# Kernel optimization log

Hardware: AMD Instinct MI355X
Metric: run time of the kernel (lower is better)

Reference implementation:

```python
import jax, jax.numpy as jnp
import numpy as np

EPS = 1e-8  # matches F.cosine_similarity eps


def setup_inputs() -> dict:
    key = jax.random.key(0)
    k1, k2 = jax.random.split(key)
    N, D = 4096, 256
    z1 = jax.random.normal(k1, (N, D), dtype=jnp.float32)
    z2 = jax.random.normal(k2, (N, D), dtype=jnp.float32)
    log_temperature = jnp.asarray(np.log(0.07), dtype=jnp.float32)
    return {"z1": z1, "z2": z2, "log_temperature": log_temperature}


def reference(z1, z2, log_temperature):
    N = z1.shape[0]
    z = jnp.concatenate([z1, z2], axis=0)                      # (2N, D)
    # cosine similarity: normalize once, then a single GEMM
    norm = jnp.maximum(jnp.linalg.norm(z, axis=-1, keepdims=True), EPS)
    zn = z / norm
    sim = zn @ zn.T                                            # (2N, 2N)
    diag = jnp.eye(2 * N, dtype=bool)
    sim = jnp.where(diag, -jnp.inf, sim)
    targets = jnp.concatenate([jnp.arange(N, 2 * N), jnp.arange(0, N)])
    logits = sim / jnp.exp(log_temperature)
    logp = jax.nn.log_softmax(logits, axis=-1)                 # (2N, 2N)
    loss = -jnp.mean(jnp.take_along_axis(logp, targets[:, None], axis=1))
    correct = jnp.sum(jnp.argmax(sim, axis=1) == targets).astype(jnp.float32) / 2.0
    return (loss, correct)
```

## Files before the change

kernel.cpp:

```cpp
#include <hip/hip_runtime.h>
#include <hip/hip_fp16.h>

#define NTOT 8192
#define NHALF 4096
#define DIM 256
#define LOG2E 1.4426950408889634f
#define NEG_BIG -1e30f
#define COLSPLIT 8
#define BM 128
#define BN 64
#define CPB (NTOT / COLSPLIT)

typedef _Float16 half8 __attribute__((ext_vector_type(8)));
typedef float floatx4 __attribute__((ext_vector_type(4)));

__global__ __launch_bounds__(256) void k_normalize(const float* __restrict__ z1,
                                                   const float* __restrict__ z2,
                                                   __half* __restrict__ zn) {
  int row = blockIdx.x * 4 + (threadIdx.x >> 6);
  int lane = threadIdx.x & 63;
  const float* src = (row < NHALF) ? (z1 + (size_t)row * DIM)
                                   : (z2 + (size_t)(row - NHALF) * DIM);
  float4 v = ((const float4*)src)[lane];
  float ss = v.x * v.x + v.y * v.y + v.z * v.z + v.w * v.w;
#pragma unroll
  for (int m = 1; m < 64; m <<= 1) ss += __shfl_xor(ss, m);
  float inv = 1.0f / fmaxf(sqrtf(ss), 1e-8f);
  __half2 h0, h1;
  h0.x = __float2half_rn(v.x * inv);
  h0.y = __float2half_rn(v.y * inv);
  h1.x = __float2half_rn(v.z * inv);
  h1.y = __float2half_rn(v.w * inv);
  __half2* dst = (__half2*)(zn + (size_t)row * DIM + lane * 4);
  dst[0] = h0;
  dst[1] = h1;
}

__global__ __launch_bounds__(256) void k_tsim(const __half* __restrict__ zn,
                                              float* __restrict__ tsim) {
  int row = blockIdx.x * 4 + (threadIdx.x >> 6);
  int lane = threadIdx.x & 63;
  int tgt = (row < NHALF) ? row + NHALF : row - NHALF;
  const __half2* a = (const __half2*)(zn + (size_t)row * DIM);
  const __half2* b = (const __half2*)(zn + (size_t)tgt * DIM);
  float s = 0.f;
#pragma unroll
  for (int j = 0; j < 2; j++) {
    float2 xf = __half22float2(a[lane * 2 + j]);
    float2 yf = __half22float2(b[lane * 2 + j]);
    s += xf.x * yf.x + xf.y * yf.y;
  }
#pragma unroll
  for (int m = 1; m < 64; m <<= 1) s += __shfl_xor(s, m);
  if (lane == 0) tsim[row] = s;
}

__global__ __launch_bounds__(256, 2) void k_main(const __half* __restrict__ zn,
                                                 const float* __restrict__ logT,
                                                 float* __restrict__ pM,
                                                 float* __restrict__ pL,
                                                 int* __restrict__ pI) {
  __shared__ uint4 lds[BN * 32];

  int bx = blockIdx.x;
  int rowTile = bx >> 3;
  int colq = bx & 7;
  int rowBase = rowTile * BM;
  int colBase = colq * CPB;
  int tid = threadIdx.x;
  int w = tid >> 6;
  int lane = tid & 63;
  int quad = lane >> 4;
  int cl = lane & 15;

  float invT = expf(-logT[0]);
  float kk = invT * LOG2E;

  half8 a[2][8];
  {
    int ar0 = rowBase + w * 32 + cl;
    int ar1 = ar0 + 16;
#pragma unroll
    for (int ks = 0; ks < 8; ks++) {
      a[0][ks] = *(const half8*)(zn + (size_t)ar0 * DIM + ks * 32 + quad * 8);
      a[1][ks] = *(const half8*)(zn + (size_t)ar1 * DIM + ks * 32 + quad * 8);
    }
  }

  float M[8], L[8];
  int AI[8];
#pragma unroll
  for (int s = 0; s < 8; s++) {
    M[s] = -3e38f;
    L[s] = 0.f;
    AI[s] = 0;
  }

  for (int t = 0; t < CPB / BN; t++) {
    __syncthreads();
#pragma unroll
    for (int i = 0; i < 8; i++) {
      int idx = tid + i * 256;
      int c = idx >> 5, ch = idx & 31;
      int g = colBase + t * BN + c;
      uint4 v = *(const uint4*)(zn + (size_t)g * DIM + ch * 8);
      lds[c * 32 + (ch ^ (c & 7))] = v;
    }
    __syncthreads();

    floatx4 acc[2][4];
#pragma unroll
    for (int rt = 0; rt < 2; rt++)
#pragma unroll
      for (int nt = 0; nt < 4; nt++) acc[rt][nt] = (floatx4){0.f, 0.f, 0.f, 0.f};

#pragma unroll
    for (int nt = 0; nt < 4; nt++) {
      int bc = nt * 16 + cl;
#pragma unroll
      for (int ks = 0; ks < 8; ks++) {
        int ch = ks * 4 + quad;
        half8 b = *(const half8*)&lds[bc * 32 + (ch ^ (bc & 7))];
        acc[0][nt] = __builtin_amdgcn_mfma_f32_16x16x32_f16(a[0][ks], b, acc[0][nt], 0, 0, 0);
        acc[1][nt] = __builtin_amdgcn_mfma_f32_16x16x32_f16(a[1][ks], b, acc[1][nt], 0, 0, 0);
      }
    }

    int colT = colBase + t * BN;
#pragma unroll
    for (int rt = 0; rt < 2; rt++) {
      int growB = rowBase + w * 32 + rt * 16 + quad * 4;
#pragma unroll
      for (int r = 0; r < 4; r++) {
        int grow = growB + r;
        float v0 = acc[rt][0][r], v1 = acc[rt][1][r];
        float v2 = acc[rt][2][r], v3 = acc[rt][3][r];
        int c0 = colT + cl;
        if (c0 == grow) v0 = NEG_BIG;
        if (c0 + 16 == grow) v1 = NEG_BIG;
        if (c0 + 32 == grow) v2 = NEG_BIG;
        if (c0 + 48 == grow) v3 = NEG_BIG;
        float mv = v0;
        int mi = c0;
        if (v1 > mv) { mv = v1; mi = c0 + 16; }
        if (v2 > mv) { mv = v2; mi = c0 + 32; }
        if (v3 > mv) { mv = v3; mi = c0 + 48; }
        int slot = rt * 4 + r;
        float Mo = M[slot];
        float Mn = fmaxf(Mo, mv);
        if (mv > Mo) AI[slot] = mi;
        float se = exp2f((v0 - Mn) * kk) + exp2f((v1 - Mn) * kk) +
                   exp2f((v2 - Mn) * kk) + exp2f((v3 - Mn) * kk);
        L[slot] = L[slot] * exp2f((Mo - Mn) * kk) + se;
        M[slot] = Mn;
      }
    }
  }

#pragma unroll
  for (int s = 0; s < 8; s++) {
    float m = M[s], l = L[s];
    int ai = AI[s];
#pragma unroll
    for (int sh = 1; sh < 16; sh <<= 1) {
      float om = __shfl_xor(m, sh);
      float ol = __shfl_xor(l, sh);
      int oi = __shfl_xor(ai, sh);
      float mn = fmaxf(m, om);
      l = l * exp2f((m - mn) * kk) + ol * exp2f((om - mn) * kk);
      if (om > m || (om == m && oi < ai)) ai = oi;
      m = mn;
    }
    M[s] = m;
    L[s] = l;
    AI[s] = ai;
  }

  if (cl == 0) {
#pragma unroll
    for (int rt = 0; rt < 2; rt++)
#pragma unroll
      for (int r = 0; r < 4; r++) {
        int grow = rowBase + w * 32 + rt * 16 + quad * 4 + r;
        int s = rt * 4 + r;
        int p = grow * COLSPLIT + colq;
        pM[p] = M[s];
        pL[p] = L[s];
        pI[p] = AI[s];
      }
  }
}

__global__ __launch_bounds__(256) void k_reduce(const float* __restrict__ pM,
                                                const float* __restrict__ pL,
                                                const int* __restrict__ pI,
                                                const float* __restrict__ tsim,
                                                const float* __restrict__ logT,
                                                float* __restrict__ out) {
  int row = blockIdx.x * 256 + threadIdx.x;
  float invT = expf(-logT[0]);
  float kk = invT * LOG2E;
  float m = -3e38f;
  int idx = 0;
#pragma unroll
  for (int q = 0; q < COLSPLIT; q++) {
    float mq = pM[row * COLSPLIT + q];
    if (mq > m) { m = mq; idx = pI[row * COLSPLIT + q]; }
  }
  float Lt = 0.f;
#pragma unroll
  for (int q = 0; q < COLSPLIT; q++)
    Lt += pL[row * COLSPLIT + q] * exp2f((pM[row * COLSPLIT + q] - m) * kk);
  int tgt = (row < NHALF) ? row + NHALF : row - NHALF;
  float logpt = (tsim[row] - m) * invT - logf(Lt);
  float loss = -logpt;
  float corr = (idx == tgt) ? 1.f : 0.f;

  __shared__ float sl[256], sc[256];
  sl[threadIdx.x] = loss;
  sc[threadIdx.x] = corr;
  __syncthreads();
  for (int s = 128; s > 0; s >>= 1) {
    if (threadIdx.x < s) {
      sl[threadIdx.x] += sl[threadIdx.x + s];
      sc[threadIdx.x] += sc[threadIdx.x + s];
    }
    __syncthreads();
  }
  if (threadIdx.x == 0) {
    atomicAdd(out + 0, sl[0] * (1.0f / (float)NTOT));
    atomicAdd(out + 1, sc[0] * 0.5f);
  }
}

extern "C" void kernel_launch(void* const* d_in, const int* in_sizes, int n_in,
                              void* d_out, int out_size, void* d_ws, size_t ws_size,
                              hipStream_t stream) {
  const float* z1 = (const float*)d_in[0];
  const float* z2 = (const float*)d_in[1];
  const float* logT = (const float*)d_in[2];
  float* out = (float*)d_out;

  char* ws = (char*)d_ws;
  __half* zn = (__half*)ws;
  float* tsim = (float*)(ws + 4 * 1024 * 1024);
  float* pM = (float*)(ws + 4 * 1024 * 1024 + 32 * 1024);
  float* pL = (float*)((char*)pM + NTOT * COLSPLIT * 4);
  int* pI = (int*)((char*)pL + NTOT * COLSPLIT * 4);

  k_normalize<<<NTOT / 4, 256, 0, stream>>>(z1, z2, zn);
  k_tsim<<<NTOT / 4, 256, 0, stream>>>(zn, tsim);
  k_main<<<(NTOT / BM) * COLSPLIT, 256, 0, stream>>>(zn, logT, pM, pL, pI);
  hipMemsetAsync(d_out, 0, 2 * sizeof(float), stream);
  k_reduce<<<NTOT / 256, 256, 0, stream>>>(pM, pL, pI, tsim, logT, out);
}
```

Measured before the change: 133.3 us.

## Fuse target-sim and final reduction into main kernel, drop online softmax rescaling

Removes the separate tsim and reduce kernels and the memset. The main kernel now captures the target similarity from its MFMA tiles and does the final reduction in the last block, chosen by an atomic counter. The online softmax becomes a plain sum of exp2(v*kk) with no running-max rescale, and argmax is replaced by a comparison of the target similarity against the row max. Tile loads move to global_load_lds direct-to-LDS copies. The unshifted exponent relies on cosine bounds to avoid overflow, and the correctness count can differ from the reference on ties.

Result: slower. 164.9 us (+23.7%).

```diff
diff --git a/kernel.cpp b/kernel.cpp
--- a/kernel.cpp
+++ b/kernel.cpp
@@ -5,18 +5,25 @@
 #define NHALF 4096
 #define DIM 256
 #define LOG2E 1.4426950408889634f
+#define LN2f 0.6931471805599453f
 #define NEG_BIG -1e30f
 #define COLSPLIT 8
 #define BM 128
 #define BN 64
 #define CPB (NTOT / COLSPLIT)
+#define NTILES (CPB / BN)
+#define NBLK ((NTOT / BM) * COLSPLIT)
 
 typedef _Float16 half8 __attribute__((ext_vector_type(8)));
 typedef float floatx4 __attribute__((ext_vector_type(4)));
+typedef const __attribute__((address_space(1))) uint4 guint4_t;
+typedef __attribute__((address_space(3))) uint4 luint4_t;
 
 __global__ __launch_bounds__(256) void k_normalize(const float* __restrict__ z1,
                                                    const float* __restrict__ z2,
-                                                   __half* __restrict__ zn) {
+                                                   __half* __restrict__ zn,
+                                                   unsigned int* __restrict__ cnt) {
+  if (blockIdx.x == 0 && threadIdx.x == 0) *cnt = 0;
   int row = blockIdx.x * 4 + (threadIdx.x >> 6);
   int lane = threadIdx.x & 63;
   const float* src = (row < NHALF) ? (z1 + (size_t)row * DIM)
@@ -36,75 +43,91 @@
   dst[1] = h1;
 }
 
-__global__ __launch_bounds__(256) void k_tsim(const __half* __restrict__ zn,
-                                              float* __restrict__ tsim) {
-  int row = blockIdx.x * 4 + (threadIdx.x >> 6);
-  int lane = threadIdx.x & 63;
-  int tgt = (row < NHALF) ? row + NHALF : row - NHALF;
-  const __half2* a = (const __half2*)(zn + (size_t)row * DIM);
-  const __half2* b = (const __half2*)(zn + (size_t)tgt * DIM);
-  float s = 0.f;
-#pragma unroll
-  for (int j = 0; j < 2; j++) {
-    float2 xf = __half22float2(a[lane * 2 + j]);
-    float2 yf = __half22float2(b[lane * 2 + j]);
-    s += xf.x * yf.x + xf.y * yf.y;
-  }
-#pragma unroll
-  for (int m = 1; m < 64; m <<= 1) s += __shfl_xor(s, m);
-  if (lane == 0) tsim[row] = s;
-}
-
-__global__ __launch_bounds__(256, 2) void k_main(const __half* __restrict__ zn,
-                                                 const float* __restrict__ logT,
-                                                 float* __restrict__ pM,
-                                                 float* __restrict__ pL,
-                                                 int* __restrict__ pI) {
+template <int MODE>
+__device__ __forceinline__ void upd(const floatx4 (&acc)[2][4], float (&Mx)[8],
+                                    float (&L)[8], float* __restrict__ tS,
+                                    int R0, int colT, int cl, int quad, int off,
+                                    float kk) {
+#pragma unroll
+  for (int rt = 0; rt < 2; rt++) {
+#pragma unroll
+    for (int r = 0; r < 4; r++) {
+      const int s = rt * 4 + r;
+      const int grow = R0 + rt * 16 + quad * 4 + r;
+      float v0 = acc[rt][0][r], v1 = acc[rt][1][r];
+      float v2 = acc[rt][2][r], v3 = acc[rt][3][r];
+      const int c0 = colT + cl;
+      if (MODE == 2) {
+        const int tc = grow + off;
+        if (c0 == tc) tS[grow] = v0;
+        if (c0 + 16 == tc) tS[grow] = v1;
+        if (c0 + 32 == tc) tS[grow] = v2;
+        if (c0 + 48 == tc) tS[grow] = v3;
+      }
+      if (MODE == 1) {
+        v0 = (c0 == grow) ? NEG_BIG : v0;
+        v1 = (c0 + 16 == grow) ? NEG_BIG : v1;
+        v2 = (c0 + 32 == grow) ? NEG_BIG : v2;
+        v3 = (c0 + 48 == grow) ? NEG_BIG : v3;
+      }
+      Mx[s] = fmaxf(fmaxf(Mx[s], fmaxf(v0, v1)), fmaxf(v2, v3));
+      L[s] += (exp2f(v0 * kk) + exp2f(v1 * kk)) + (exp2f(v2 * kk) + exp2f(v3 * kk));
+    }
+  }
+}
+
+__global__ __launch_bounds__(256, 2) void k_main(
+    const __half* __restrict__ zn, const float* __restrict__ logT,
+    float* __restrict__ tS, float* __restrict__ pM, float* __restrict__ pL,
+    unsigned int* __restrict__ cnt, float* __restrict__ out) {
   __shared__ uint4 lds[BN * 32];
-
-  int bx = blockIdx.x;
-  int rowTile = bx >> 3;
-  int colq = bx & 7;
-  int rowBase = rowTile * BM;
-  int colBase = colq * CPB;
-  int tid = threadIdx.x;
-  int w = tid >> 6;
-  int lane = tid & 63;
-  int quad = lane >> 4;
-  int cl = lane & 15;
-
-  float invT = expf(-logT[0]);
-  float kk = invT * LOG2E;
+  __shared__ int lastFlag;
+
+  const int bid = blockIdx.x;
+  const int rowTile = bid >> 3;
+  const int colq = bid & 7;
+  const int rowBase = rowTile * BM;
+  const int colBase = colq * CPB;
+  const int tid = threadIdx.x;
+  const int w = tid >> 6;
+  const int lane = tid & 63;
+  const int quad = lane >> 4;
+  const int cl = lane & 15;
+
+  const float invT = expf(-logT[0]);
+  const float kk = invT * LOG2E;
+
+  const int R0 = rowBase + w * 32;
+  const int off = (R0 < NHALF) ? NHALF : -NHALF;
 
   half8 a[2][8];
-  {
-    int ar0 = rowBase + w * 32 + cl;
-    int ar1 = ar0 + 16;
-#pragma unroll
-    for (int ks = 0; ks < 8; ks++) {
-      a[0][ks] = *(const half8*)(zn + (size_t)ar0 * DIM + ks * 32 + quad * 8);
-      a[1][ks] = *(const half8*)(zn + (size_t)ar1 * DIM + ks * 32 + quad * 8);
-    }
-  }
-
-  float M[8], L[8];
-  int AI[8];
-#pragma unroll
-  for (int s = 0; s < 8; s++) {
-    M[s] = -3e38f;
-    L[s] = 0.f;
-    AI[s] = 0;
-  }
-
-  for (int t = 0; t < CPB / BN; t++) {
+#pragma unroll
+  for (int ks = 0; ks < 8; ks++) {
+    a[0][ks] = *(const half8*)(zn + (size_t)(R0 + cl) * DIM + ks * 32 + quad * 8);
+    a[1][ks] = *(const half8*)(zn + (size_t)(R0 + 16 + cl) * DIM + ks * 32 + quad * 8);
+  }
+
+  const __half* gsrc[8];
+#pragma unroll
+  for (int i = 0; i < 8; i++) {
+    const int idx = i * 256 + tid;
+    const int c = idx >> 5;
+    const int ch = (idx & 31) ^ (c & 7);
+    gsrc[i] = zn + (size_t)c * DIM + ch * 8;
+  }
+
+  float Mx[8], L[8];
+#pragma unroll
+  for (int s = 0; s < 8; s++) { Mx[s] = NEG_BIG; L[s] = 0.f; }
+
+  for (int t = 0; t < NTILES; t++) {
     __syncthreads();
+    const size_t tileOff = (size_t)(colBase + t * BN) * DIM;
 #pragma unroll
     for (int i = 0; i < 8; i++) {
-      int idx = tid + i * 256;
-      int c = idx >> 5, ch = idx & 31;
-      int g = colBase + t * BN + c;
-      uint4 v = *(const uint4*)(zn + (size_t)g * DIM + ch * 8);
-      lds[c * 32 + (ch ^ (c & 7))] = v;
+      const __half* gp = gsrc[i] + tileOff;
+      __builtin_amdgcn_global_load_lds((guint4_t*)(const void*)gp,
+                                       (luint4_t*)&lds[i * 256 + w * 64], 16, 0, 0);
     }
     __syncthreads();
 
@@ -116,120 +139,83 @@
 
 #pragma unroll
     for (int nt = 0; nt < 4; nt++) {
-      int bc = nt * 16 + cl;
+      const int bc = nt * 16 + cl;
 #pragma unroll
       for (int ks = 0; ks < 8; ks++) {
-        int ch = ks * 4 + quad;
+        const int ch = ks * 4 + quad;
         half8 b = *(const half8*)&lds[bc * 32 + (ch ^ (bc & 7))];
         acc[0][nt] = __builtin_amdgcn_mfma_f32_16x16x32_f16(a[0][ks], b, acc[0][nt], 0, 0, 0);
         acc[1][nt] = __builtin_amdgcn_mfma_f32_16x16x32_f16(a[1][ks], b, acc[1][nt], 0, 0, 0);
       }
     }
 
-    int colT = colBase + t * BN;
-#pragma unroll
-    for (int rt = 0; rt < 2; rt++) {
-      int growB = rowBase + w * 32 + rt * 16 + quad * 4;
+    const int colT = colBase + t * BN;
+    const bool diagHit = (R0 < colT + BN) && (colT < R0 + 32);
+    const int T0 = R0 + off;
+    const bool tgtHit = (T0 < colT + BN) && (colT < T0 + 32);
+    if (diagHit)      upd<1>(acc, Mx, L, tS, R0, colT, cl, quad, off, kk);
+    else if (tgtHit)  upd<2>(acc, Mx, L, tS, R0, colT, cl, quad, off, kk);
+    else              upd<0>(acc, Mx, L, tS, R0, colT, cl, quad, off, kk);
+  }
+
+#pragma unroll
+  for (int s = 0; s < 8; s++) {
+    float m = Mx[s], l = L[s];
+#pragma unroll
+    for (int sh = 1; sh < 16; sh <<= 1) {
+      m = fmaxf(m, __shfl_xor(m, sh));
+      l += __shfl_xor(l, sh);
+    }
+    Mx[s] = m;
+    L[s] = l;
+  }
+  if (cl == 0) {
+#pragma unroll
+    for (int rt = 0; rt < 2; rt++)
 #pragma unroll
       for (int r = 0; r < 4; r++) {
-        int grow = growB + r;
-        float v0 = acc[rt][0][r], v1 = acc[rt][1][r];
-        float v2 = acc[rt][2][r], v3 = acc[rt][3][r];
-        int c0 = colT + cl;
-        if (c0 == grow) v0 = NEG_BIG;
-        if (c0 + 16 == grow) v1 = NEG_BIG;
-        if (c0 + 32 == grow) v2 = NEG_BIG;
-        if (c0 + 48 == grow) v3 = NEG_BIG;
-        float mv = v0;
-        int mi = c0;
-        if (v1 > mv) { mv = v1; mi = c0 + 16; }
-        if (v2 > mv) { mv = v2; mi = c0 + 32; }
-        if (v3 > mv) { mv = v3; mi = c0 + 48; }
-        int slot = rt * 4 + r;
-        float Mo = M[slot];
-        float Mn = fmaxf(Mo, mv);
-        if (mv > Mo) AI[slot] = mi;
-        float se = exp2f((v0 - Mn) * kk) + exp2f((v1 - Mn) * kk) +
-                   exp2f((v2 - Mn) * kk) + exp2f((v3 - Mn) * kk);
-        L[slot] = L[slot] * exp2f((Mo - Mn) * kk) + se;
-        M[slot] = Mn;
-      }
-    }
-  }
-
-#pragma unroll
-  for (int s = 0; s < 8; s++) {
-    float m = M[s], l = L[s];
-    int ai = AI[s];
-#pragma unroll
-    for (int sh = 1; sh < 16; sh <<= 1) {
-      float om = __shfl_xor(m, sh);
-      float ol = __shfl_xor(l, sh);
-      int oi = __shfl_xor(ai, sh);
-      float mn = fmaxf(m, om);
-      l = l * exp2f((m - mn) * kk) + ol * exp2f((om - mn) * kk);
-      if (om > m || (om == m && oi < ai)) ai = oi;
-      m = mn;
-    }
-    M[s] = m;
-    L[s] = l;
-    AI[s] = ai;
-  }
-
-  if (cl == 0) {
-#pragma unroll
-    for (int rt = 0; rt < 2; rt++)
-#pragma unroll
-      for (int r = 0; r < 4; r++) {
-        int grow = rowBase + w * 32 + rt * 16 + quad * 4 + r;
-        int s = rt * 4 + r;
-        int p = grow * COLSPLIT + colq;
-        pM[p] = M[s];
-        pL[p] = L[s];
-        pI[p] = AI[s];
-      }
-  }
-}
-
-__global__ __launch_bounds__(256) void k_reduce(const float* __restrict__ pM,
-                                                const float* __restrict__ pL,
-                                                const int* __restrict__ pI,
-                                                const float* __restrict__ tsim,
-                                                const float* __restrict__ logT,
-                                                float* __restrict__ out) {
-  int row = blockIdx.x * 256 + threadIdx.x;
-  float invT = expf(-logT[0]);
-  float kk = invT * LOG2E;
-  float m = -3e38f;
-  int idx = 0;
-#pragma unroll
-  for (int q = 0; q < COLSPLIT; q++) {
-    float mq = pM[row * COLSPLIT + q];
-    if (mq > m) { m = mq; idx = pI[row * COLSPLIT + q]; }
-  }
-  float Lt = 0.f;
-#pragma unroll
-  for (int q = 0; q < COLSPLIT; q++)
-    Lt += pL[row * COLSPLIT + q] * exp2f((pM[row * COLSPLIT + q] - m) * kk);
-  int tgt = (row < NHALF) ? row + NHALF : row - NHALF;
-  float logpt = (tsim[row] - m) * invT - logf(Lt);
-  float loss = -logpt;
-  float corr = (idx == tgt) ? 1.f : 0.f;
-
-  __shared__ float sl[256], sc[256];
-  sl[threadIdx.x] = loss;
-  sc[threadIdx.x] = corr;
+        const int grow = R0 + rt * 16 + quad * 4 + r;
+        const int s = rt * 4 + r;
+        pM[colq * NTOT + grow] = Mx[s];
+        pL[colq * NTOT + grow] = L[s];
+      }
+  }
+
+  __threadfence();
   __syncthreads();
-  for (int s = 128; s > 0; s >>= 1) {
-    if (threadIdx.x < s) {
-      sl[threadIdx.x] += sl[threadIdx.x + s];
-      sc[threadIdx.x] += sc[threadIdx.x + s];
-    }
+  if (tid == 0) {
+    unsigned prev = __hip_atomic_fetch_add(cnt, 1u, __ATOMIC_ACQ_REL,
+                                           __HIP_MEMORY_SCOPE_AGENT);
+    lastFlag = (prev == (unsigned)(NBLK - 1)) ? 1 : 0;
+  }
+  __syncthreads();
+  if (!lastFlag) return;
+
+  float lossSum = 0.f, corrSum = 0.f;
+  for (int rr = 0; rr < NTOT / 256; rr++) {
+    const int row = rr * 256 + tid;
+    float m = NEG_BIG, Lr = 0.f;
+#pragma unroll
+    for (int q = 0; q < COLSPLIT; q++) {
+      m = fmaxf(m, pM[q * NTOT + row]);
+      Lr += pL[q * NTOT + row];
+    }
+    const float tp = tS[row];
+    lossSum += LN2f * log2f(Lr) - tp * invT;
+    corrSum += (tp >= m) ? 1.f : 0.f;
+  }
+  float* sl = (float*)lds;
+  float* sc = sl + 256;
+  sl[tid] = lossSum;
+  sc[tid] = corrSum;
+  __syncthreads();
+  for (int s2 = 128; s2 > 0; s2 >>= 1) {
+    if (tid < s2) { sl[tid] += sl[tid + s2]; sc[tid] += sc[tid + s2]; }
     __syncthreads();
   }
-  if (threadIdx.x == 0) {
-    atomicAdd(out + 0, sl[0] * (1.0f / (float)NTOT));
-    atomicAdd(out + 1, sc[0] * 0.5f);
+  if (tid == 0) {
+    out[0] = sl[0] * (1.0f / (float)NTOT);
+    out[1] = sc[0] * 0.5f;
   }
 }
 
@@ -239,18 +225,14 @@
   const float* z1 = (const float*)d_in[0];
   const float* z2 = (const float*)d_in[1];
   const float* logT = (const float*)d_in[2];
-  float* out = (float*)d_out;
 
   char* ws = (char*)d_ws;
   __half* zn = (__half*)ws;
-  float* tsim = (float*)(ws + 4 * 1024 * 1024);
-  float* pM = (float*)(ws + 4 * 1024 * 1024 + 32 * 1024);
-  float* pL = (float*)((char*)pM + NTOT * COLSPLIT * 4);
-  int* pI = (int*)((char*)pL + NTOT * COLSPLIT * 4);
-
-  k_normalize<<<NTOT / 4, 256, 0, stream>>>(z1, z2, zn);
-  k_tsim<<<NTOT / 4, 256, 0, stream>>>(zn, tsim);
-  k_main<<<(NTOT / BM) * COLSPLIT, 256, 0, stream>>>(zn, logT, pM, pL, pI);
-  hipMemsetAsync(d_out, 0, 2 * sizeof(float), stream);
-  k_reduce<<<NTOT / 256, 256, 0, stream>>>(pM, pL, pI, tsim, logT, out);
-}
+  float* tS = (float*)(ws + (size_t)(4 << 20));
+  float* pM = (float*)(ws + (size_t)(4 << 20) + (32 << 10));
+  float* pL = pM + COLSPLIT * NTOT;
+  unsigned int* cnt = (unsigned int*)(pL + COLSPLIT * NTOT);
+
+  k_normalize<<<NTOT / 4, 256, 0, stream>>>(z1, z2, zn, cnt);
+  k_main<<<NBLK, 256, 0, stream>>>(zn, logT, tS, pM, pL, cnt, (float*)d_out);
+}
```

## Fuse normalize with target-sim and fold final reduction into main kernel

Applied to the files above, without the earlier changes.

Normalization and the positive-pair similarity are now computed together in one kernel, with each thread pair handling a row of z1 and its matching row of z2. The target similarity is taken from fp32 dot products rather than fp16 normalized vectors. The separate reduce kernel and the memset are replaced by a last-block-done pattern in the main kernel, using an atomic counter and threadfence. This cuts the number of launches from five to two, but the final reduction now runs serially over 8192 rows inside a single block.

Result: slower. 241.4 us (+81.0%).

```diff
diff --git a/kernel.cpp b/kernel.cpp
--- a/kernel.cpp
+++ b/kernel.cpp
@@ -10,57 +10,64 @@
 #define BM 128
 #define BN 64
 #define CPB (NTOT / COLSPLIT)
+#define NBLK ((NTOT / BM) * COLSPLIT)
 
 typedef _Float16 half8 __attribute__((ext_vector_type(8)));
 typedef float floatx4 __attribute__((ext_vector_type(4)));
 
-__global__ __launch_bounds__(256) void k_normalize(const float* __restrict__ z1,
+__global__ __launch_bounds__(256) void k_norm_tsim(const float* __restrict__ z1,
                                                    const float* __restrict__ z2,
-                                                   __half* __restrict__ zn) {
+                                                   __half* __restrict__ zn,
+                                                   float* __restrict__ tsim,
+                                                   unsigned int* __restrict__ cnt) {
+  if (blockIdx.x == 0 && threadIdx.x == 0) *cnt = 0;
   int row = blockIdx.x * 4 + (threadIdx.x >> 6);
   int lane = threadIdx.x & 63;
-  const float* src = (row < NHALF) ? (z1 + (size_t)row * DIM)
-                                   : (z2 + (size_t)(row - NHALF) * DIM);
-  float4 v = ((const float4*)src)[lane];
-  float ss = v.x * v.x + v.y * v.y + v.z * v.z + v.w * v.w;
-#pragma unroll
-  for (int m = 1; m < 64; m <<= 1) ss += __shfl_xor(ss, m);
-  float inv = 1.0f / fmaxf(sqrtf(ss), 1e-8f);
-  __half2 h0, h1;
-  h0.x = __float2half_rn(v.x * inv);
-  h0.y = __float2half_rn(v.y * inv);
-  h1.x = __float2half_rn(v.z * inv);
-  h1.y = __float2half_rn(v.w * inv);
-  __half2* dst = (__half2*)(zn + (size_t)row * DIM + lane * 4);
-  dst[0] = h0;
-  dst[1] = h1;
-}
-
-__global__ __launch_bounds__(256) void k_tsim(const __half* __restrict__ zn,
-                                              float* __restrict__ tsim) {
-  int row = blockIdx.x * 4 + (threadIdx.x >> 6);
-  int lane = threadIdx.x & 63;
-  int tgt = (row < NHALF) ? row + NHALF : row - NHALF;
-  const __half2* a = (const __half2*)(zn + (size_t)row * DIM);
-  const __half2* b = (const __half2*)(zn + (size_t)tgt * DIM);
-  float s = 0.f;
-#pragma unroll
-  for (int j = 0; j < 2; j++) {
-    float2 xf = __half22float2(a[lane * 2 + j]);
-    float2 yf = __half22float2(b[lane * 2 + j]);
-    s += xf.x * yf.x + xf.y * yf.y;
-  }
-#pragma unroll
-  for (int m = 1; m < 64; m <<= 1) s += __shfl_xor(s, m);
-  if (lane == 0) tsim[row] = s;
+  float4 va = ((const float4*)(z1 + (size_t)row * DIM))[lane];
+  float4 vb = ((const float4*)(z2 + (size_t)row * DIM))[lane];
+  float ssa = va.x * va.x + va.y * va.y + va.z * va.z + va.w * va.w;
+  float ssb = vb.x * vb.x + vb.y * vb.y + vb.z * vb.z + vb.w * vb.w;
+  float sab = va.x * vb.x + va.y * vb.y + va.z * vb.z + va.w * vb.w;
+#pragma unroll
+  for (int m = 1; m < 64; m <<= 1) {
+    ssa += __shfl_xor(ssa, m);
+    ssb += __shfl_xor(ssb, m);
+    sab += __shfl_xor(sab, m);
+  }
+  float inva = 1.0f / fmaxf(sqrtf(ssa), 1e-8f);
+  float invb = 1.0f / fmaxf(sqrtf(ssb), 1e-8f);
+  __half2 a0, a1, b0, b1;
+  a0.x = __float2half_rn(va.x * inva);
+  a0.y = __float2half_rn(va.y * inva);
+  a1.x = __float2half_rn(va.z * inva);
+  a1.y = __float2half_rn(va.w * inva);
+  b0.x = __float2half_rn(vb.x * invb);
+  b0.y = __float2half_rn(vb.y * invb);
+  b1.x = __float2half_rn(vb.z * invb);
+  b1.y = __float2half_rn(vb.w * invb);
+  __half2* da = (__half2*)(zn + (size_t)row * DIM + lane * 4);
+  __half2* db = (__half2*)(zn + (size_t)(row + NHALF) * DIM + lane * 4);
+  da[0] = a0;
+  da[1] = a1;
+  db[0] = b0;
+  db[1] = b1;
+  if (lane == 0) {
+    float t = sab * inva * invb;
+    tsim[row] = t;
+    tsim[row + NHALF] = t;
+  }
 }
 
 __global__ __launch_bounds__(256, 2) void k_main(const __half* __restrict__ zn,
                                                  const float* __restrict__ logT,
                                                  float* __restrict__ pM,
                                                  float* __restrict__ pL,
-                                                 int* __restrict__ pI) {
+                                                 int* __restrict__ pI,
+                                                 const float* __restrict__ tsim,
+                                                 unsigned int* __restrict__ cnt,
+                                                 float* __restrict__ out) {
   __shared__ uint4 lds[BN * 32];
+  __shared__ int lastFlag;
 
   int bx = blockIdx.x;
   int rowTile = bx >> 3;
@@ -189,47 +196,48 @@
         pI[p] = AI[s];
       }
   }
-}
-
-__global__ __launch_bounds__(256) void k_reduce(const float* __restrict__ pM,
-                                                const float* __restrict__ pL,
-                                                const int* __restrict__ pI,
-                                                const float* __restrict__ tsim,
-                                                const float* __restrict__ logT,
-                                                float* __restrict__ out) {
-  int row = blockIdx.x * 256 + threadIdx.x;
-  float invT = expf(-logT[0]);
-  float kk = invT * LOG2E;
-  float m = -3e38f;
-  int idx = 0;
-#pragma unroll
-  for (int q = 0; q < COLSPLIT; q++) {
-    float mq = pM[row * COLSPLIT + q];
-    if (mq > m) { m = mq; idx = pI[row * COLSPLIT + q]; }
-  }
-  float Lt = 0.f;
-#pragma unroll
-  for (int q = 0; q < COLSPLIT; q++)
-    Lt += pL[row * COLSPLIT + q] * exp2f((pM[row * COLSPLIT + q] - m) * kk);
-  int tgt = (row < NHALF) ? row + NHALF : row - NHALF;
-  float logpt = (tsim[row] - m) * invT - logf(Lt);
-  float loss = -logpt;
-  float corr = (idx == tgt) ? 1.f : 0.f;
-
-  __shared__ float sl[256], sc[256];
-  sl[threadIdx.x] = loss;
-  sc[threadIdx.x] = corr;
+
+  __threadfence();
   __syncthreads();
-  for (int s = 128; s > 0; s >>= 1) {
-    if (threadIdx.x < s) {
-      sl[threadIdx.x] += sl[threadIdx.x + s];
-      sc[threadIdx.x] += sc[threadIdx.x + s];
-    }
+  if (tid == 0) {
+    unsigned prev = __hip_atomic_fetch_add(cnt, 1u, __ATOMIC_ACQ_REL,
+                                           __HIP_MEMORY_SCOPE_AGENT);
+    lastFlag = (prev == (unsigned)(NBLK - 1)) ? 1 : 0;
+  }
+  __syncthreads();
+  if (!lastFlag) return;
+
+  float lossSum = 0.f, corrSum = 0.f;
+  for (int rr = 0; rr < NTOT / 256; rr++) {
+    int row = rr * 256 + tid;
+    float m = -3e38f;
+    int idx = 0;
+#pragma unroll
+    for (int q = 0; q < COLSPLIT; q++) {
+      float mq = pM[row * COLSPLIT + q];
+      if (mq > m) { m = mq; idx = pI[row * COLSPLIT + q]; }
+    }
+    float Lt = 0.f;
+#pragma unroll
+    for (int q = 0; q < COLSPLIT; q++)
+      Lt += pL[row * COLSPLIT + q] * exp2f((pM[row * COLSPLIT + q] - m) * kk);
+    int tgt = (row < NHALF) ? row + NHALF : row - NHALF;
+    float logpt = (tsim[row] - m) * invT - logf(Lt);
+    lossSum += -logpt;
+    corrSum += (idx == tgt) ? 1.f : 0.f;
+  }
+  float* sl = (float*)lds;
+  float* sc = sl + 256;
+  sl[tid] = lossSum;
+  sc[tid] = corrSum;
+  __syncthreads();
+  for (int s2 = 128; s2 > 0; s2 >>= 1) {
+    if (tid < s2) { sl[tid] += sl[tid + s2]; sc[tid] += sc[tid + s2]; }
     __syncthreads();
   }
-  if (threadIdx.x == 0) {
-    atomicAdd(out + 0, sl[0] * (1.0f / (float)NTOT));
-    atomicAdd(out + 1, sc[0] * 0.5f);
+  if (tid == 0) {
+    out[0] = sl[0] * (1.0f / (float)NTOT);
+    out[1] = sc[0] * 0.5f;
   }
 }
 
@@ -239,18 +247,15 @@
   const float* z1 = (const float*)d_in[0];
   const float* z2 = (const float*)d_in[1];
   const float* logT = (const float*)d_in[2];
-  float* out = (float*)d_out;
 
   char* ws = (char*)d_ws;
   __half* zn = (__half*)ws;
-  float* tsim = (float*)(ws + 4 * 1024 * 1024);
-  float* pM = (float*)(ws + 4 * 1024 * 1024 + 32 * 1024);
-  float* pL = (float*)((char*)pM + NTOT * COLSPLIT * 4);
-  int* pI = (int*)((char*)pL + NTOT * COLSPLIT * 4);
-
-  k_normalize<<<NTOT / 4, 256, 0, stream>>>(z1, z2, zn);
-  k_tsim<<<NTOT / 4, 256, 0, stream>>>(zn, tsim);
-  k_main<<<(NTOT / BM) * COLSPLIT, 256, 0, stream>>>(zn, logT, pM, pL, pI);
-  hipMemsetAsync(d_out, 0, 2 * sizeof(float), stream);
-  k_reduce<<<NTOT / 256, 256, 0, stream>>>(pM, pL, pI, tsim, logT, out);
+  float* tsim = (float*)(ws + (size_t)(4 << 20));
+  float* pM = (float*)(ws + (size_t)(4 << 20) + (32 << 10));
+  float* pL = pM + NTOT * COLSPLIT;
+  int* pI = (int*)(pL + NTOT * COLSPLIT);
+  unsigned int* cnt = (unsigned int*)(pI + NTOT * COLSPLIT);
+
+  k_norm_tsim<<<NHALF / 4, 256, 0, stream>>>(z1, z2, zn, tsim, cnt);
+  k_main<<<NBLK, 256, 0, stream>>>(zn, logT, pM, pL, pI, tsim, cnt, (float*)d_out);
 }
```
